# Kernel optimization log

Hardware: AMD Instinct MI355X
Metric: run time of the kernel (lower is better)

## Reference

```python
import jax, jax.numpy as jnp
import numpy as np

N_NODES = 100000
HIDDEN = 128
N_CLASSES = 8


def _sage_conv(x, src, dst, Wl, bl, Wr, num_nodes):
    # PyG SAGEConv (aggr='mean'): out = lin_l(mean_{j in N(i)} x_j) + lin_r(x_i)
    agg = jax.ops.segment_sum(x[src], dst, num_segments=num_nodes)          # [N, H]
    deg = jax.ops.segment_sum(jnp.ones((src.shape[0],), x.dtype), dst,
                              num_segments=num_nodes)                       # [N]
    mean = agg / jnp.maximum(deg, 1.0)[:, None]
    return mean @ Wl + bl + x @ Wr


def setup_inputs() -> dict:
    key = jax.random.key(0)
    ks = jax.random.split(key, 12)
    s = 1.0 / np.sqrt(HIDDEN)
    inp = {
        "node_emb": jax.random.normal(ks[0], (N_NODES, HIDDEN), jnp.float32),
        "Wl0": jax.random.normal(ks[1], (HIDDEN, HIDDEN), jnp.float32) * s,
        "bl0": jnp.zeros((HIDDEN,), jnp.float32),
        "Wr0": jax.random.normal(ks[2], (HIDDEN, HIDDEN), jnp.float32) * s,
        "Wl1": jax.random.normal(ks[3], (HIDDEN, HIDDEN), jnp.float32) * s,
        "bl1": jnp.zeros((HIDDEN,), jnp.float32),
        "Wr1": jax.random.normal(ks[4], (HIDDEN, HIDDEN), jnp.float32) * s,
        "mlp_W1": jax.random.normal(ks[5], (2 * HIDDEN, HIDDEN), jnp.float32) * (1.0 / np.sqrt(2 * HIDDEN)),
        "mlp_b1": jnp.zeros((HIDDEN,), jnp.float32),
        "mlp_W2": jax.random.normal(ks[6], (HIDDEN, N_CLASSES), jnp.float32) * s,
        "mlp_b2": jnp.zeros((N_CLASSES,), jnp.float32),
        "edge_index": jax.random.randint(ks[7], (2, 1600000), 0, N_NODES, jnp.int64),
        "edge_q": jax.random.randint(ks[8], (2, 500000), 0, N_NODES, jnp.int64),
    }
    return inp


def reference(node_emb, Wl0, bl0, Wr0, Wl1, bl1, Wr1,
              mlp_W1, mlp_b1, mlp_W2, mlp_b2, edge_index, edge_q):
    src, dst = edge_index[0], edge_index[1]
    n = node_emb.shape[0]
    # layer 0 + relu (dropout is identity in eval / p=0)
    x = jax.nn.relu(_sage_conv(node_emb, src, dst, Wl0, bl0, Wr0, n))
    # layer 1 + relu
    x = jax.nn.relu(_sage_conv(x, src, dst, Wl1, bl1, Wr1, n))
    # edge classifier: gather endpoint pairs, concat, 2-layer MLP
    qs, qd = edge_q[0], edge_q[1]
    edge_feat = jnp.concatenate([x[qs], x[qd]], axis=-1)   # [Eq, 2H]
    h = jax.nn.relu(edge_feat @ mlp_W1 + mlp_b1)
    logits = h @ mlp_W2 + mlp_b2                            # [Eq, C]
    return logits
```

## Files before the change

kernel.cpp:

```cpp
#include <hip/hip_runtime.h>
#include <hip/hip_bf16.h>
#include <cstdint>
#include <cstddef>

#define HID 128
#define SH 9
#define NODES_PER_BIN 512

typedef __attribute__((ext_vector_type(8))) __bf16 bf16x8;
typedef __attribute__((ext_vector_type(4))) float floatx4;

__device__ __forceinline__ ushort f2bf(float f) {
    uint u = __float_as_uint(f);
    u += 0x7fff + ((u >> 16) & 1);
    return (ushort)(u >> 16);
}
__device__ __forceinline__ float bf2f(uint h) { return __uint_as_float(h << 16); }
__device__ __forceinline__ uint pack2(float a, float b) {
    return (uint)f2bf(a) | ((uint)f2bf(b) << 16);
}

__device__ __forceinline__ void async16(const ushort* g, ushort* l) {
    __builtin_amdgcn_global_load_lds(
        (const __attribute__((address_space(1))) uint*)g,
        (__attribute__((address_space(3))) uint*)l, 16, 0, 0);
}


__global__ void k_hist(const int* __restrict__ dst, int E, int* __restrict__ binc) {
    __shared__ int h[256];
    int t = threadIdx.x;
    h[t] = 0;
    __syncthreads();
    for (int e = blockIdx.x * 256 + t; e < E; e += gridDim.x * 256)
        atomicAdd(&h[dst[e] >> SH], 1);
    __syncthreads();
    if (h[t]) atomicAdd(&binc[t], h[t]);
}

__global__ void k_binscan(const int* __restrict__ binc, int* __restrict__ bin_start,
                          int* __restrict__ bin_cursor, int E) {
    __shared__ int s[256];
    int t = threadIdx.x;
    int c = binc[t];
    s[t] = c;
    __syncthreads();
    #pragma unroll
    for (int off = 1; off < 256; off <<= 1) {
        int add = (t >= off) ? s[t - off] : 0;
        __syncthreads();
        s[t] += add;
        __syncthreads();
    }
    int excl = s[t] - c;
    bin_start[t] = excl;
    bin_cursor[t] = excl;
    if (t == 255) bin_start[256] = E;
}

__global__ __launch_bounds__(256) void k_part(
    const int* __restrict__ src, const int* __restrict__ dst, int E,
    int* __restrict__ bin_cursor, uint* __restrict__ ebuf) {
    __shared__ int h[256];
    __shared__ int sc[256];
    __shared__ int rk[256];
    __shared__ int gb[256];
    __shared__ uint2 ro[2048];
    int t = threadIdx.x;
    int base = blockIdx.x * 2048;
    h[t] = 0;
    __syncthreads();
    int dd[8], ss[8];
    bool ok[8];
    #pragma unroll
    for (int k = 0; k < 8; ++k) {
        int e = base + k * 256 + t;
        ok[k] = e < E;
        if (ok[k]) {
            dd[k] = dst[e];
            ss[k] = src[e];
            atomicAdd(&h[dd[k] >> SH], 1);
        }
    }
    __syncthreads();
    sc[t] = h[t];
    __syncthreads();
    #pragma unroll
    for (int off = 1; off < 256; off <<= 1) {
        int add = (t >= off) ? sc[t - off] : 0;
        __syncthreads();
        sc[t] += add;
        __syncthreads();
    }
    rk[t] = sc[t] - h[t];
    {
        int c = h[t];
        if (c > 0) gb[t] = atomicAdd(&bin_cursor[t], c);
    }
    __syncthreads();
    #pragma unroll
    for (int k = 0; k < 8; ++k) {
        if (ok[k]) {
            int bin = dd[k] >> SH;
            int r = atomicAdd(&rk[bin], 1);
            ro[r] = make_uint2((uint)dd[k],
                               ((uint)(dd[k] & (NODES_PER_BIN - 1)) << 23) | (uint)ss[k]);
        }
    }
    __syncthreads();
    int nv = sc[255];
    for (int i = t; i < nv; i += 256) {
        uint2 pr = ro[i];
        int bin = (int)(pr.x >> SH);
        int excl = sc[bin] - h[bin];
        ebuf[gb[bin] + (i - excl)] = pr.y;
    }
}

__global__ __launch_bounds__(256) void k_csr(
    const uint* __restrict__ ebuf, const int* __restrict__ bin_start,
    int* __restrict__ rowptr, int* __restrict__ csr, int N, int E, int NB) {
    __shared__ int cnt[512];
    __shared__ int p[256];
    __shared__ int excl[512];
    int t = threadIdx.x;
    int b = blockIdx.x;
    int d0 = b << SH;
    int ebase = bin_start[b], eend = bin_start[b + 1];
    cnt[t] = 0; cnt[t + 256] = 0;
    __syncthreads();
    for (int e = ebase + t; e < eend; e += 256)
        atomicAdd(&cnt[ebuf[e] >> 23], 1);
    __syncthreads();
    p[t] = cnt[2 * t] + cnt[2 * t + 1];
    __syncthreads();
    #pragma unroll
    for (int off = 1; off < 256; off <<= 1) {
        int add = (t >= off) ? p[t - off] : 0;
        __syncthreads();
        p[t] += add;
        __syncthreads();
    }
    int e0 = (t == 0) ? 0 : p[t - 1];
    excl[2 * t] = e0;
    excl[2 * t + 1] = e0 + cnt[2 * t];
    __syncthreads();
    #pragma unroll
    for (int i = t; i < 512; i += 256) {
        int node = d0 + i;
        if (node < N) rowptr[node] = ebase + excl[i];
    }
    if (b == NB - 1 && t == 0) rowptr[N] = E;
    __syncthreads();
    for (int e = ebase + t; e < eend; e += 256) {
        uint w = ebuf[e];
        int r = atomicAdd(&excl[w >> 23], 1);
        csr[ebase + r] = (int)(w & 0x7FFFFFu);
    }
}


__global__ void k_cvt(const float* __restrict__ in, ushort* __restrict__ out, int n4) {
    int i = blockIdx.x * blockDim.x + threadIdx.x;
    if (i < n4) {
        float4 v = ((const float4*)in)[i];
        ((uint2*)out)[i] = make_uint2(pack2(v.x, v.y), pack2(v.z, v.w));
    }
}

__global__ void k_prepw(const float* __restrict__ Wl0, const float* __restrict__ Wr0,
                        const float* __restrict__ Wl1, const float* __restrict__ Wr1,
                        const float* __restrict__ W1,  const float* __restrict__ W2,
                        ushort* __restrict__ WlrT0, ushort* __restrict__ WlrT1,
                        ushort* __restrict__ W1T,   ushort* __restrict__ W2T) {
    int idx = blockIdx.x * 256 + threadIdx.x;
    if (idx < 32768) {
        int n = idx >> 8, k = idx & 255;
        float v = (k < 128) ? Wl0[k * 128 + n] : Wr0[(k - 128) * 128 + n];
        WlrT0[n * 256 + k] = f2bf(v);
    } else if (idx < 65536) {
        int t = idx - 32768; int n = t >> 8, k = t & 255;
        float v = (k < 128) ? Wl1[k * 128 + n] : Wr1[(k - 128) * 128 + n];
        WlrT1[n * 256 + k] = f2bf(v);
    } else if (idx < 98304) {
        int t = idx - 65536; int n = t >> 8, k = t & 255;
        W1T[n * 256 + k] = f2bf(W1[k * 128 + n]);
    } else if (idx < 100352) {
        int t = idx - 98304; int n = t >> 7, k = t & 127;
        W2T[n * 128 + k] = (n < 8) ? f2bf(W2[k * 8 + n]) : (ushort)0;
    }
}

__global__ __launch_bounds__(256) void k_agg4(const ushort* __restrict__ x,
                                              const int* __restrict__ rowptr,
                                              const int* __restrict__ csr,
                                              ushort* __restrict__ mean, int N) {
    int node = blockIdx.x * 16 + (threadIdx.x >> 4);
    if (node >= N) return;
    int u = threadIdx.x & 15;
    int b = rowptr[node], e = rowptr[node + 1];
    const uint4* xv = (const uint4*)x;
    float a0=0.f,a1=0.f,a2=0.f,a3=0.f,a4=0.f,a5=0.f,a6=0.f,a7=0.f;
    int j = b;
    for (; j + 3 < e; j += 4) {
        int s0 = csr[j], s1 = csr[j+1], s2 = csr[j+2], s3 = csr[j+3];
        uint4 v0 = xv[(size_t)s0 * 16 + u];
        uint4 v1 = xv[(size_t)s1 * 16 + u];
        uint4 v2 = xv[(size_t)s2 * 16 + u];
        uint4 v3 = xv[(size_t)s3 * 16 + u];
        a0 += __uint_as_float(v0.x << 16) + __uint_as_float(v1.x << 16)
            + __uint_as_float(v2.x << 16) + __uint_as_float(v3.x << 16);
        a1 += __uint_as_float(v0.x & 0xffff0000u) + __uint_as_float(v1.x & 0xffff0000u)
            + __uint_as_float(v2.x & 0xffff0000u) + __uint_as_float(v3.x & 0xffff0000u);
        a2 += __uint_as_float(v0.y << 16) + __uint_as_float(v1.y << 16)
            + __uint_as_float(v2.y << 16) + __uint_as_float(v3.y << 16);
        a3 += __uint_as_float(v0.y & 0xffff0000u) + __uint_as_float(v1.y & 0xffff0000u)
            + __uint_as_float(v2.y & 0xffff0000u) + __uint_as_float(v3.y & 0xffff0000u);
        a4 += __uint_as_float(v0.z << 16) + __uint_as_float(v1.z << 16)
            + __uint_as_float(v2.z << 16) + __uint_as_float(v3.z << 16);
        a5 += __uint_as_float(v0.z & 0xffff0000u) + __uint_as_float(v1.z & 0xffff0000u)
            + __uint_as_float(v2.z & 0xffff0000u) + __uint_as_float(v3.z & 0xffff0000u);
        a6 += __uint_as_float(v0.w << 16) + __uint_as_float(v1.w << 16)
            + __uint_as_float(v2.w << 16) + __uint_as_float(v3.w << 16);
        a7 += __uint_as_float(v0.w & 0xffff0000u) + __uint_as_float(v1.w & 0xffff0000u)
            + __uint_as_float(v2.w & 0xffff0000u) + __uint_as_float(v3.w & 0xffff0000u);
    }
    for (; j < e; ++j) {
        uint4 v = xv[(size_t)csr[j] * 16 + u];
        a0 += __uint_as_float(v.x << 16);
        a1 += __uint_as_float(v.x & 0xffff0000u);
        a2 += __uint_as_float(v.y << 16);
        a3 += __uint_as_float(v.y & 0xffff0000u);
        a4 += __uint_as_float(v.z << 16);
        a5 += __uint_as_float(v.z & 0xffff0000u);
        a6 += __uint_as_float(v.w << 16);
        a7 += __uint_as_float(v.w & 0xffff0000u);
    }
    float inv = 1.f / fmaxf((float)(e - b), 1.f);
    uint4 o;
    o.x = pack2(a0 * inv, a1 * inv);
    o.y = pack2(a2 * inv, a3 * inv);
    o.z = pack2(a4 * inv, a5 * inv);
    o.w = pack2(a6 * inv, a7 * inv);
    ((uint4*)mean)[(size_t)node * 16 + u] = o;
}

__global__ __launch_bounds__(256) void k_gemm16(
    const ushort* __restrict__ Alo, const ushort* __restrict__ Ahi,
    const ushort* __restrict__ WT, const float* __restrict__ bias,
    ushort* __restrict__ out, int M) {
    __shared__ ushort As[4096];
    __shared__ ushort Bs[4096];
    int tid = threadIdx.x;
    int l = tid & 63, w = tid >> 6;
    int i0 = blockIdx.x * 128;
    int c0 = w * 64 + l, c1 = c0 + 256;
    int rA0 = c0 >> 2, sA0 = (c0 & 3) * 8;
    int rA1 = c1 >> 2, sA1 = (c1 & 3) * 8;
    int g0 = i0 + rA0; if (g0 >= M) g0 = M - 1;
    int g1 = i0 + rA1; if (g1 >= M) g1 = M - 1;
    int lm = l & 15, lq = l >> 4;

    floatx4 acc[2][8];
    #pragma unroll
    for (int rt = 0; rt < 2; rt++)
        #pragma unroll
        for (int ct = 0; ct < 8; ct++) acc[rt][ct] = (floatx4){0.f, 0.f, 0.f, 0.f};

    for (int kt = 0; kt < 8; ++kt) {
        const ushort* Asrc = (kt < 4) ? Alo : Ahi;
        int kb = (kt & 3) * 32;
        async16(Asrc + (size_t)g0 * 128 + kb + sA0, As + w * 512);
        async16(Asrc + (size_t)g1 * 128 + kb + sA1, As + 2048 + w * 512);
        async16(WT + rA0 * 256 + kt * 32 + sA0, Bs + w * 512);
        async16(WT + rA1 * 256 + kt * 32 + sA1, Bs + 2048 + w * 512);
        __syncthreads();
        bf16x8 a0 = *(const bf16x8*)(As + (w * 32 + lm) * 32 + lq * 8);
        bf16x8 a1 = *(const bf16x8*)(As + (w * 32 + 16 + lm) * 32 + lq * 8);
        #pragma unroll
        for (int ct = 0; ct < 8; ++ct) {
            bf16x8 b = *(const bf16x8*)(Bs + (ct * 16 + lm) * 32 + lq * 8);
            acc[0][ct] = __builtin_amdgcn_mfma_f32_16x16x32_bf16(a0, b, acc[0][ct], 0, 0, 0);
            acc[1][ct] = __builtin_amdgcn_mfma_f32_16x16x32_bf16(a1, b, acc[1][ct], 0, 0, 0);
        }
        __syncthreads();
    }

    float bv[8];
    #pragma unroll
    for (int ct = 0; ct < 8; ++ct) bv[ct] = bias[ct * 16 + lm];
    #pragma unroll
    for (int rt = 0; rt < 2; ++rt)
        #pragma unroll
        for (int ct = 0; ct < 8; ++ct)
            #pragma unroll
            for (int r = 0; r < 4; ++r) {
                int grow = i0 + w * 32 + rt * 16 + lq * 4 + r;
                if (grow < M)
                    out[(size_t)grow * 128 + ct * 16 + lm] =
                        f2bf(fmaxf(acc[rt][ct][r] + bv[ct], 0.f));
            }
}

#define HSTR 136

__global__ __launch_bounds__(256) void k_mlp(
    const ushort* __restrict__ x16, const int* __restrict__ qs, const int* __restrict__ qd,
    const ushort* __restrict__ W1T, const float* __restrict__ b1,
    const ushort* __restrict__ W2T, const float* __restrict__ b2,
    float* __restrict__ out, int Eq) {
    __shared__ union {
        struct { ushort As[4096]; ushort Bs[4096]; } s1;
        struct { ushort Hs[128 * HSTR]; ushort W2s[16 * HSTR]; } s2;
    } sm;
    __shared__ int Ns[256];
    int tid = threadIdx.x;
    int l = tid & 63, w = tid >> 6;
    int lm = l & 15, lq = l >> 4;
    int e0 = blockIdx.x * 128;
    {
        int r = tid & 127;
        int e = e0 + r; if (e >= Eq) e = Eq - 1;
        Ns[tid] = (tid < 128) ? qs[e] : qd[e];
    }
    __syncthreads();

    int c0 = w * 64 + l, c1 = c0 + 256;
    int rA0 = c0 >> 2, sA0 = (c0 & 3) * 8;
    int rA1 = c1 >> 2, sA1 = (c1 & 3) * 8;
    ushort* As = sm.s1.As;
    ushort* Bs = sm.s1.Bs;

    floatx4 acc[2][8];
    #pragma unroll
    for (int rt = 0; rt < 2; rt++)
        #pragma unroll
        for (int ct = 0; ct < 8; ct++) acc[rt][ct] = (floatx4){0.f, 0.f, 0.f, 0.f};

    for (int kt = 0; kt < 8; ++kt) {
        int kb = (kt & 3) * 32;
        const int* Nbase = (kt < 4) ? Ns : (Ns + 128);
        int n0 = Nbase[rA0], n1 = Nbase[rA1];
        async16(x16 + (size_t)n0 * 128 + kb + sA0, As + w * 512);
        async16(x16 + (size_t)n1 * 128 + kb + sA1, As + 2048 + w * 512);
        async16(W1T + rA0 * 256 + kt * 32 + sA0, Bs + w * 512);
        async16(W1T + rA1 * 256 + kt * 32 + sA1, Bs + 2048 + w * 512);
        __syncthreads();
        bf16x8 a0 = *(const bf16x8*)(As + (w * 32 + lm) * 32 + lq * 8);
        bf16x8 a1 = *(const bf16x8*)(As + (w * 32 + 16 + lm) * 32 + lq * 8);
        #pragma unroll
        for (int ct = 0; ct < 8; ++ct) {
            bf16x8 b = *(const bf16x8*)(Bs + (ct * 16 + lm) * 32 + lq * 8);
            acc[0][ct] = __builtin_amdgcn_mfma_f32_16x16x32_bf16(a0, b, acc[0][ct], 0, 0, 0);
            acc[1][ct] = __builtin_amdgcn_mfma_f32_16x16x32_bf16(a1, b, acc[1][ct], 0, 0, 0);
        }
        __syncthreads();
    }

    float b1v[8];
    #pragma unroll
    for (int ct = 0; ct < 8; ++ct) b1v[ct] = b1[ct * 16 + lm];
    #pragma unroll
    for (int rt = 0; rt < 2; ++rt)
        #pragma unroll
        for (int ct = 0; ct < 8; ++ct)
            #pragma unroll
            for (int r = 0; r < 4; ++r) {
                int row = w * 32 + rt * 16 + lq * 4 + r;
                int col = ct * 16 + lm;
                sm.s2.Hs[row * HSTR + col] = f2bf(fmaxf(acc[rt][ct][r] + b1v[ct], 0.f));
            }
    {
        int n = tid >> 4, kc = (tid & 15) * 8;
        #pragma unroll
        for (int j = 0; j < 8; ++j)
            sm.s2.W2s[n * HSTR + kc + j] = W2T[n * 128 + kc + j];
    }
    __syncthreads();

    floatx4 acc2[2];
    acc2[0] = (floatx4){0.f, 0.f, 0.f, 0.f};
    acc2[1] = (floatx4){0.f, 0.f, 0.f, 0.f};
    #pragma unroll
    for (int ks = 0; ks < 4; ++ks) {
        bf16x8 bw = *(const bf16x8*)(sm.s2.W2s + lm * HSTR + ks * 32 + lq * 8);
        bf16x8 h0 = *(const bf16x8*)(sm.s2.Hs + (w * 32 + lm) * HSTR + ks * 32 + lq * 8);
        bf16x8 h1 = *(const bf16x8*)(sm.s2.Hs + (w * 32 + 16 + lm) * HSTR + ks * 32 + lq * 8);
        acc2[0] = __builtin_amdgcn_mfma_f32_16x16x32_bf16(h0, bw, acc2[0], 0, 0, 0);
        acc2[1] = __builtin_amdgcn_mfma_f32_16x16x32_bf16(h1, bw, acc2[1], 0, 0, 0);
    }
    if (lm < 8) {
        float bb = b2[lm];
        #pragma unroll
        for (int rt = 0; rt < 2; ++rt)
            #pragma unroll
            for (int r = 0; r < 4; ++r) {
                int eg = e0 + w * 32 + rt * 16 + lq * 4 + r;
                if (eg < Eq) out[(size_t)eg * 8 + lm] = acc2[rt][r] + bb;
            }
    }
}


extern "C" void kernel_launch(void* const* d_in, const int* in_sizes, int n_in,
                              void* d_out, int out_size, void* d_ws, size_t ws_size,
                              hipStream_t stream) {
    const float* node_emb = (const float*)d_in[0];
    const float* Wl0 = (const float*)d_in[1];
    const float* bl0 = (const float*)d_in[2];
    const float* Wr0 = (const float*)d_in[3];
    const float* Wl1 = (const float*)d_in[4];
    const float* bl1 = (const float*)d_in[5];
    const float* Wr1 = (const float*)d_in[6];
    const float* W1  = (const float*)d_in[7];
    const float* b1  = (const float*)d_in[8];
    const float* W2  = (const float*)d_in[9];
    const float* b2  = (const float*)d_in[10];
    const int* eidx  = (const int*)d_in[11];
    const int* eq    = (const int*)d_in[12];

    int N  = in_sizes[0] / HID;
    int E  = in_sizes[11] / 2;
    int Eq = in_sizes[12] / 2;
    const int* srcp = eidx;
    const int* dstp = eidx + E;
    const int* qs = eq;
    const int* qd = eq + Eq;
    float* outp = (float*)d_out;
    int NB = (N + NODES_PER_BIN - 1) >> SH;

    char* ws = (char*)d_ws;
    size_t off = 0;
    auto take = [&](size_t bytes) -> char* {
        char* p = ws + off;
        off += (bytes + 255) & ~(size_t)255;
        return p;
    };
    int* binc       = (int*)take(256 * 4);
    int* bin_start  = (int*)take(257 * 4);
    int* bin_cursor = (int*)take(256 * 4);
    int* rowptr     = (int*)take((size_t)(N + 1) * 4);
    int* csr        = (int*)take((size_t)E * 4);
    char* meanreg   = take((size_t)N * HID * 2);
    uint* ebuf      = (uint*)meanreg;
    ushort* mean16  = (ushort*)meanreg;
    ushort* x0_16   = (ushort*)take((size_t)N * HID * 2);
    ushort* xa16    = (ushort*)take((size_t)N * HID * 2);
    ushort* xb16    = x0_16;
    ushort* WlrT0   = (ushort*)take(32768 * 2);
    ushort* WlrT1   = (ushort*)take(32768 * 2);
    ushort* W1T     = (ushort*)take(32768 * 2);
    ushort* W2T     = (ushort*)take(2048 * 2);

    hipMemsetAsync(binc, 0, 256 * 4, stream);

    k_hist<<<256, 256, 0, stream>>>(dstp, E, binc);
    k_binscan<<<1, 256, 0, stream>>>(binc, bin_start, bin_cursor, E);
    int pb = (E + 2047) / 2048;
    k_part<<<pb, 256, 0, stream>>>(srcp, dstp, E, bin_cursor, ebuf);
    k_csr<<<NB, 256, 0, stream>>>(ebuf, bin_start, rowptr, csr, N, E, NB);

    int n4 = N * HID / 4;
    const int TB = 256;
    k_cvt<<<(n4 + TB - 1) / TB, TB, 0, stream>>>(node_emb, x0_16, n4);
    k_prepw<<<392, 256, 0, stream>>>(Wl0, Wr0, Wl1, Wr1, W1, W2, WlrT0, WlrT1, W1T, W2T);

    int ag = (N + 15) / 16;
    int mg = (N + 127) / 128;
    k_agg4<<<ag, 256, 0, stream>>>(x0_16, rowptr, csr, mean16, N);
    k_gemm16<<<mg, 256, 0, stream>>>(mean16, x0_16, WlrT0, bl0, xa16, N);
    k_agg4<<<ag, 256, 0, stream>>>(xa16, rowptr, csr, mean16, N);
    k_gemm16<<<mg, 256, 0, stream>>>(mean16, xa16, WlrT1, bl1, xb16, N);

    int eg = (Eq + 127) / 128;
    k_mlp<<<eg, 256, 0, stream>>>(xb16, qs, qd, W1T, b1, W2T, b2, outp, Eq);
}
```

Measured before the change: 391.1 us.

## Precompute per-node MLP first-layer projections and reduce edge MLP to gather-add

Splits the first MLP layer algebraically: concat(x[qs],x[qd])@W1 = x[qs]@W1_top + x[qd]@W1_bot, so a node-level GEMM computes both halves once for all 100k nodes into a bf16 YY buffer. A new edge kernel then gathers two 128-wide rows per query edge, adds bias, applies ReLU and does the tiny 128x8 second layer with FMAs and shuffle reductions. This replaces 500k-row GEMM work with a 100k-row GEMM (two column halves) plus a gather, at the cost of an extra N x 256 bf16 write/read and extra bf16 rounding of the pre-activation sums. Workspace is reorganized so xa16 and YY share a region with mean16.

Measured after the change: 430.1 us. 1.1x slower.

```diff
diff --git a/kernel.cpp b/kernel.cpp
--- a/kernel.cpp
+++ b/kernel.cpp
@@ -170,9 +170,9 @@
 
 __global__ void k_prepw(const float* __restrict__ Wl0, const float* __restrict__ Wr0,
                         const float* __restrict__ Wl1, const float* __restrict__ Wr1,
-                        const float* __restrict__ W1,  const float* __restrict__ W2,
+                        const float* __restrict__ W1,
                         ushort* __restrict__ WlrT0, ushort* __restrict__ WlrT1,
-                        ushort* __restrict__ W1T,   ushort* __restrict__ W2T) {
+                        ushort* __restrict__ W1T) {
     int idx = blockIdx.x * 256 + threadIdx.x;
     if (idx < 32768) {
         int n = idx >> 8, k = idx & 255;
@@ -185,9 +185,6 @@
     } else if (idx < 98304) {
         int t = idx - 65536; int n = t >> 8, k = t & 255;
         W1T[n * 256 + k] = f2bf(W1[k * 128 + n]);
-    } else if (idx < 100352) {
-        int t = idx - 98304; int n = t >> 7, k = t & 127;
-        W2T[n * 128 + k] = (n < 8) ? f2bf(W2[k * 8 + n]) : (ushort)0;
     }
 }
 
@@ -302,34 +299,22 @@
             }
 }
 
-#define HSTR 136
-
-__global__ __launch_bounds__(256) void k_mlp(
-    const ushort* __restrict__ x16, const int* __restrict__ qs, const int* __restrict__ qd,
-    const ushort* __restrict__ W1T, const float* __restrict__ b1,
-    const ushort* __restrict__ W2T, const float* __restrict__ b2,
-    float* __restrict__ out, int Eq) {
-    __shared__ union {
-        struct { ushort As[4096]; ushort Bs[4096]; } s1;
-        struct { ushort Hs[128 * HSTR]; ushort W2s[16 * HSTR]; } s2;
-    } sm;
-    __shared__ int Ns[256];
+__global__ __launch_bounds__(256) void k_gemmYY(
+    const ushort* __restrict__ X, const ushort* __restrict__ W1T,
+    ushort* __restrict__ YY, int M) {
+    __shared__ ushort As[4096];
+    __shared__ ushort Bs[4096];
     int tid = threadIdx.x;
     int l = tid & 63, w = tid >> 6;
-    int lm = l & 15, lq = l >> 4;
-    int e0 = blockIdx.x * 128;
-    {
-        int r = tid & 127;
-        int e = e0 + r; if (e >= Eq) e = Eq - 1;
-        Ns[tid] = (tid < 128) ? qs[e] : qd[e];
-    }
-    __syncthreads();
-
+    int i0 = blockIdx.x * 128;
+    int y = blockIdx.y;
+    const ushort* WT = W1T + y * 128;
     int c0 = w * 64 + l, c1 = c0 + 256;
     int rA0 = c0 >> 2, sA0 = (c0 & 3) * 8;
     int rA1 = c1 >> 2, sA1 = (c1 & 3) * 8;
-    ushort* As = sm.s1.As;
-    ushort* Bs = sm.s1.Bs;
+    int g0 = i0 + rA0; if (g0 >= M) g0 = M - 1;
+    int g1 = i0 + rA1; if (g1 >= M) g1 = M - 1;
+    int lm = l & 15, lq = l >> 4;
 
     floatx4 acc[2][8];
     #pragma unroll
@@ -337,14 +322,12 @@
         #pragma unroll
         for (int ct = 0; ct < 8; ct++) acc[rt][ct] = (floatx4){0.f, 0.f, 0.f, 0.f};
 
-    for (int kt = 0; kt < 8; ++kt) {
-        int kb = (kt & 3) * 32;
-        const int* Nbase = (kt < 4) ? Ns : (Ns + 128);
-        int n0 = Nbase[rA0], n1 = Nbase[rA1];
-        async16(x16 + (size_t)n0 * 128 + kb + sA0, As + w * 512);
-        async16(x16 + (size_t)n1 * 128 + kb + sA1, As + 2048 + w * 512);
-        async16(W1T + rA0 * 256 + kt * 32 + sA0, Bs + w * 512);
-        async16(W1T + rA1 * 256 + kt * 32 + sA1, Bs + 2048 + w * 512);
+    for (int kt = 0; kt < 4; ++kt) {
+        int kb = kt * 32;
+        async16(X + (size_t)g0 * 128 + kb + sA0, As + w * 512);
+        async16(X + (size_t)g1 * 128 + kb + sA1, As + 2048 + w * 512);
+        async16(WT + rA0 * 256 + kb + sA0, Bs + w * 512);
+        async16(WT + rA1 * 256 + kb + sA1, Bs + 2048 + w * 512);
         __syncthreads();
         bf16x8 a0 = *(const bf16x8*)(As + (w * 32 + lm) * 32 + lq * 8);
         bf16x8 a1 = *(const bf16x8*)(As + (w * 32 + 16 + lm) * 32 + lq * 8);
@@ -357,47 +340,70 @@
         __syncthreads();
     }
 
-    float b1v[8];
-    #pragma unroll
-    for (int ct = 0; ct < 8; ++ct) b1v[ct] = b1[ct * 16 + lm];
     #pragma unroll
     for (int rt = 0; rt < 2; ++rt)
         #pragma unroll
         for (int ct = 0; ct < 8; ++ct)
             #pragma unroll
             for (int r = 0; r < 4; ++r) {
-                int row = w * 32 + rt * 16 + lq * 4 + r;
-                int col = ct * 16 + lm;
-                sm.s2.Hs[row * HSTR + col] = f2bf(fmaxf(acc[rt][ct][r] + b1v[ct], 0.f));
+                int grow = i0 + w * 32 + rt * 16 + lq * 4 + r;
+                if (grow < M)
+                    YY[(size_t)grow * 256 + y * 128 + ct * 16 + lm] =
+                        f2bf(acc[rt][ct][r]);
             }
-    {
-        int n = tid >> 4, kc = (tid & 15) * 8;
-        #pragma unroll
-        for (int j = 0; j < 8; ++j)
-            sm.s2.W2s[n * HSTR + kc + j] = W2T[n * 128 + kc + j];
-    }
-    __syncthreads();
-
-    floatx4 acc2[2];
-    acc2[0] = (floatx4){0.f, 0.f, 0.f, 0.f};
-    acc2[1] = (floatx4){0.f, 0.f, 0.f, 0.f};
-    #pragma unroll
-    for (int ks = 0; ks < 4; ++ks) {
-        bf16x8 bw = *(const bf16x8*)(sm.s2.W2s + lm * HSTR + ks * 32 + lq * 8);
-        bf16x8 h0 = *(const bf16x8*)(sm.s2.Hs + (w * 32 + lm) * HSTR + ks * 32 + lq * 8);
-        bf16x8 h1 = *(const bf16x8*)(sm.s2.Hs + (w * 32 + 16 + lm) * HSTR + ks * 32 + lq * 8);
-        acc2[0] = __builtin_amdgcn_mfma_f32_16x16x32_bf16(h0, bw, acc2[0], 0, 0, 0);
-        acc2[1] = __builtin_amdgcn_mfma_f32_16x16x32_bf16(h1, bw, acc2[1], 0, 0, 0);
-    }
-    if (lm < 8) {
-        float bb = b2[lm];
-        #pragma unroll
-        for (int rt = 0; rt < 2; ++rt)
+}
+
+__global__ __launch_bounds__(256) void k_edge(
+    const uint4* __restrict__ YY, const int* __restrict__ qs, const int* __restrict__ qd,
+    const float* __restrict__ W2, const float* __restrict__ b1,
+    const float* __restrict__ b2, float* __restrict__ out, int Eq) {
+    int u = threadIdx.x & 15;
+    int g = (blockIdx.x * 256 + threadIdx.x) >> 4;
+    int nG = (gridDim.x * 256) >> 4;
+
+    float w2r[8][8];
+    float b1r[8];
+    #pragma unroll
+    for (int j = 0; j < 8; ++j) {
+        float4 w0 = *(const float4*)(W2 + (u * 8 + j) * 8);
+        float4 w1 = *(const float4*)(W2 + (u * 8 + j) * 8 + 4);
+        w2r[j][0] = w0.x; w2r[j][1] = w0.y; w2r[j][2] = w0.z; w2r[j][3] = w0.w;
+        w2r[j][4] = w1.x; w2r[j][5] = w1.y; w2r[j][6] = w1.z; w2r[j][7] = w1.w;
+        b1r[j] = b1[u * 8 + j];
+    }
+    float4 bsel = (u & 1) ? *(const float4*)(b2 + 4) : *(const float4*)b2;
+
+    for (int e = g; e < Eq; e += nG) {
+        int ns = qs[e], nd = qd[e];
+        uint4 vs = YY[(size_t)ns * 32 + u];
+        uint4 vd = YY[(size_t)nd * 32 + 16 + u];
+        float p[8] = {0.f, 0.f, 0.f, 0.f, 0.f, 0.f, 0.f, 0.f};
+        uint sv[4] = {vs.x, vs.y, vs.z, vs.w};
+        uint dv[4] = {vd.x, vd.y, vd.z, vd.w};
+        #pragma unroll
+        for (int q = 0; q < 4; ++q) {
+            float hl = __uint_as_float(sv[q] << 16) + __uint_as_float(dv[q] << 16)
+                     + b1r[2 * q];
+            float hh = __uint_as_float(sv[q] & 0xffff0000u)
+                     + __uint_as_float(dv[q] & 0xffff0000u) + b1r[2 * q + 1];
+            hl = fmaxf(hl, 0.f);
+            hh = fmaxf(hh, 0.f);
             #pragma unroll
-            for (int r = 0; r < 4; ++r) {
-                int eg = e0 + w * 32 + rt * 16 + lq * 4 + r;
-                if (eg < Eq) out[(size_t)eg * 8 + lm] = acc2[rt][r] + bb;
-            }
+            for (int c = 0; c < 8; ++c)
+                p[c] = fmaf(hl, w2r[2 * q][c], fmaf(hh, w2r[2 * q + 1][c], p[c]));
+        }
+        #pragma unroll
+        for (int m = 1; m <= 8; m <<= 1)
+            #pragma unroll
+            for (int c = 0; c < 8; ++c) p[c] += __shfl_xor(p[c], m);
+        if (u < 2) {
+            float4 o;
+            o.x = p[u * 4 + 0] + bsel.x;
+            o.y = p[u * 4 + 1] + bsel.y;
+            o.z = p[u * 4 + 2] + bsel.z;
+            o.w = p[u * 4 + 3] + bsel.w;
+            *(float4*)(out + (size_t)e * 8 + u * 4) = o;
+        }
     }
 }
 
@@ -441,16 +447,16 @@
     int* bin_cursor = (int*)take(256 * 4);
     int* rowptr     = (int*)take((size_t)(N + 1) * 4);
     int* csr        = (int*)take((size_t)E * 4);
-    char* meanreg   = take((size_t)N * HID * 2);
-    uint* ebuf      = (uint*)meanreg;
-    ushort* mean16  = (ushort*)meanreg;
+    char* R         = take((size_t)N * HID * 4);
+    uint* ebuf      = (uint*)R;
+    ushort* mean16  = (ushort*)R;
+    ushort* xa16    = (ushort*)(R + (size_t)N * HID * 2);
+    ushort* YY      = (ushort*)R;
     ushort* x0_16   = (ushort*)take((size_t)N * HID * 2);
-    ushort* xa16    = (ushort*)take((size_t)N * HID * 2);
     ushort* xb16    = x0_16;
     ushort* WlrT0   = (ushort*)take(32768 * 2);
     ushort* WlrT1   = (ushort*)take(32768 * 2);
     ushort* W1T     = (ushort*)take(32768 * 2);
-    ushort* W2T     = (ushort*)take(2048 * 2);
 
     hipMemsetAsync(binc, 0, 256 * 4, stream);
 
@@ -463,7 +469,7 @@
     int n4 = N * HID / 4;
     const int TB = 256;
     k_cvt<<<(n4 + TB - 1) / TB, TB, 0, stream>>>(node_emb, x0_16, n4);
-    k_prepw<<<392, 256, 0, stream>>>(Wl0, Wr0, Wl1, Wr1, W1, W2, WlrT0, WlrT1, W1T, W2T);
+    k_prepw<<<384, 256, 0, stream>>>(Wl0, Wr0, Wl1, Wr1, W1, WlrT0, WlrT1, W1T);
 
     int ag = (N + 15) / 16;
     int mg = (N + 127) / 128;
@@ -472,6 +478,6 @@
     k_agg4<<<ag, 256, 0, stream>>>(xa16, rowptr, csr, mean16, N);
     k_gemm16<<<mg, 256, 0, stream>>>(mean16, xa16, WlrT1, bl1, xb16, N);
 
-    int eg = (Eq + 127) / 128;
-    k_mlp<<<eg, 256, 0, stream>>>(xb16, qs, qd, W1T, b1, W2T, b2, outp, Eq);
-}
+    k_gemmYY<<<dim3(mg, 2), 256, 0, stream>>>(xb16, W1T, YY, N);
+    k_edge<<<1024, 256, 0, stream>>>((const uint4*)YY, qs, qd, W2, b1, b2, outp, Eq);
+}
```

## Prefetch full edge feature tile into LDS once and read W1 from global

Applied to the files above, without the earlier changes.

The MLP kernel now gathers the whole 128x256 concatenated endpoint feature tile into LDS with one batch of async loads, using an XOR-swizzled layout so later reads avoid bank conflicts. This removes the eight per-k-step load/sync rounds. The W1 operand is read straight from global memory (cache-resident) instead of being staged through LDS. In exchange, LDS use grows to 64 KB per block, which may lower occupancy, and the B-operand reads now go through the cache hierarchy rather than shared memory.

After: 486.5 us. +24.4%, slower.

```diff
diff --git a/kernel.cpp b/kernel.cpp
--- a/kernel.cpp
+++ b/kernel.cpp
@@ -310,7 +310,7 @@
     const ushort* __restrict__ W2T, const float* __restrict__ b2,
     float* __restrict__ out, int Eq) {
     __shared__ union {
-        struct { ushort As[4096]; ushort Bs[4096]; } s1;
+        ushort As[128 * 256];
         struct { ushort Hs[128 * HSTR]; ushort W2s[16 * HSTR]; } s2;
     } sm;
     __shared__ int Ns[256];
@@ -325,11 +325,16 @@
     }
     __syncthreads();
 
-    int c0 = w * 64 + l, c1 = c0 + 256;
-    int rA0 = c0 >> 2, sA0 = (c0 & 3) * 8;
-    int rA1 = c1 >> 2, sA1 = (c1 & 3) * 8;
-    ushort* As = sm.s1.As;
-    ushort* Bs = sm.s1.Bs;
+    #pragma unroll
+    for (int i = 0; i < 16; ++i) {
+        int f = i * 256 + w * 64 + l;
+        int r = f >> 5;
+        int sg = f & 31;
+        int node = Ns[((sg >> 4) << 7) | r];
+        const ushort* g = x16 + (size_t)node * 128 + (((sg & 15) ^ (r & 15)) << 3);
+        async16(g, sm.As + (i * 256 + w * 64) * 8);
+    }
+    __syncthreads();
 
     floatx4 acc[2][8];
     #pragma unroll
@@ -337,29 +342,26 @@
         #pragma unroll
         for (int ct = 0; ct < 8; ct++) acc[rt][ct] = (floatx4){0.f, 0.f, 0.f, 0.f};
 
+    int r0 = w * 32 + lm, r1 = r0 + 16;
+    #pragma unroll 2
     for (int kt = 0; kt < 8; ++kt) {
-        int kb = (kt & 3) * 32;
-        const int* Nbase = (kt < 4) ? Ns : (Ns + 128);
-        int n0 = Nbase[rA0], n1 = Nbase[rA1];
-        async16(x16 + (size_t)n0 * 128 + kb + sA0, As + w * 512);
-        async16(x16 + (size_t)n1 * 128 + kb + sA1, As + 2048 + w * 512);
-        async16(W1T + rA0 * 256 + kt * 32 + sA0, Bs + w * 512);
-        async16(W1T + rA1 * 256 + kt * 32 + sA1, Bs + 2048 + w * 512);
-        __syncthreads();
-        bf16x8 a0 = *(const bf16x8*)(As + (w * 32 + lm) * 32 + lq * 8);
-        bf16x8 a1 = *(const bf16x8*)(As + (w * 32 + 16 + lm) * 32 + lq * 8);
+        int sgl = kt * 4 + lq;
+        int ep = sgl >> 4, si = sgl & 15;
+        int seg = (ep << 4) | (si ^ lm);
+        bf16x8 a0 = *(const bf16x8*)(sm.As + r0 * 256 + seg * 8);
+        bf16x8 a1 = *(const bf16x8*)(sm.As + r1 * 256 + seg * 8);
         #pragma unroll
         for (int ct = 0; ct < 8; ++ct) {
-            bf16x8 b = *(const bf16x8*)(Bs + (ct * 16 + lm) * 32 + lq * 8);
+            bf16x8 b = *(const bf16x8*)(W1T + (ct * 16 + lm) * 256 + kt * 32 + lq * 8);
             acc[0][ct] = __builtin_amdgcn_mfma_f32_16x16x32_bf16(a0, b, acc[0][ct], 0, 0, 0);
             acc[1][ct] = __builtin_amdgcn_mfma_f32_16x16x32_bf16(a1, b, acc[1][ct], 0, 0, 0);
         }
-        __syncthreads();
     }
 
     float b1v[8];
     #pragma unroll
     for (int ct = 0; ct < 8; ++ct) b1v[ct] = b1[ct * 16 + lm];
+    __syncthreads();
     #pragma unroll
     for (int rt = 0; rt < 2; ++rt)
         #pragma unroll
```
